# Kernel optimization log

Measured on AMD Instinct MI355X. Metric: run time of the kernel, lower is better.

## Reference

```python
import jax, jax.numpy as jnp
import numpy as np
import math

# HMS 10-20 montage probe ordering and bipolar probe groups
PROBES = ["Fp1","F3","C3","P3","F7","T3","T5","O1","Fz","Cz","Pz",
          "Fp2","F4","C4","P4","F8","T4","T6","O2","EKG"]
PROBE2IDX = {p: i for i, p in enumerate(PROBES)}
PROBE_GROUPS = {
    "LL": ["Fp1","F7","T3","T5","O1"],
    "LP": ["Fp1","F3","C3","P3","O1"],
    "RP": ["Fp2","F8","T4","T6","O2"],
    "RL": ["Fp2","F4","C4","P4","O2"],
    "Z":  ["Fz","Cz","Pz"],
}
_pairs = []
for _, probes in PROBE_GROUPS.items():
    for p1, p2 in zip(probes[:-1], probes[1:]):
        _pairs.append((PROBE2IDX[p1], PROBE2IDX[p2]))
P1_IDX = np.array([p for p, _ in _pairs])  # (18,)
P2_IDX = np.array([q for _, q in _pairs])  # (18,)

SAMPLING_RATE = 40.0
HP_CUTOFF = 0.5
LP_CUTOFF = 50.0
Q = 0.7071067811865476  # torchaudio default

def _highpass_coeffs(sr, fc, q=Q):
    w0 = 2.0 * math.pi * fc / sr
    alpha = math.sin(w0) / (2.0 * q)
    c = math.cos(w0)
    b0, b1, b2 = (1 + c) / 2, -(1 + c), (1 + c) / 2
    a0, a1, a2 = 1 + alpha, -2 * c, 1 - alpha
    return (b0 / a0, b1 / a0, b2 / a0, a1 / a0, a2 / a0)

def _lowpass_coeffs(sr, fc, q=Q):
    w0 = 2.0 * math.pi * fc / sr
    alpha = math.sin(w0) / (2.0 * q)
    c = math.cos(w0)
    b0, b1, b2 = (1 - c) / 2, 1 - c, (1 - c) / 2
    a0, a1, a2 = 1 + alpha, -2 * c, 1 - alpha
    return (b0 / a0, b1 / a0, b2 / a0, a1 / a0, a2 / a0)

def _biquad(x, coeffs):
    # x: (B, C, T); direct-form-I IIR with zero initial conditions (as torchaudio lfilter)
    b0, b1, b2, a1, a2 = coeffs
    xT = jnp.moveaxis(x, -1, 0)  # (T, B, C)
    z = jnp.zeros_like(xT[0])
    def step(carry, xn):
        x1, x2, y1, y2 = carry
        yn = b0 * xn + b1 * x1 + b2 * x2 - a1 * y1 - a2 * y2
        return (xn, x1, yn, y1), yn
    _, yT = jax.lax.scan(step, (z, z, z, z), xT)
    return jnp.moveaxis(yT, 0, -1)

def setup_inputs() -> dict:
    key = jax.random.key(0)
    k1, k2 = jax.random.split(key)
    B, T, P = 128, 16384, 20
    x = jax.random.normal(k1, (B, T, P), dtype=jnp.float32)
    mask = jax.random.uniform(k2, (B, T, P), dtype=jnp.float32)
    return {"x": x, "mask": mask}

def reference(x, mask):
    # bipolar channel differences + pair masks, then (B, C=18, T)
    x_diff = x[..., P1_IDX] - x[..., P2_IDX]          # (B, T, 18)
    pair_mask = mask[..., P1_IDX] * mask[..., P2_IDX] # (B, T, 18)
    eegs = jnp.transpose(x_diff * pair_mask, (0, 2, 1))      # apply_mask=True -> (B, 18, T)
    eeg_masks = jnp.transpose(pair_mask, (0, 2, 1))          # (B, 18, T)
    eegs = _biquad(eegs, _highpass_coeffs(SAMPLING_RATE, HP_CUTOFF))
    eegs = _biquad(eegs, _lowpass_coeffs(SAMPLING_RATE, LP_CUTOFF))
    return eegs, eeg_masks
```

## Files before the change

kernel.cpp:

```cpp
#include <hip/hip_runtime.h>
#include <math.h>

#ifndef M_PI
#define M_PI 3.14159265358979323846
#endif

#define BB     128
#define TT     16384
#define PP     20
#define NCH    18
#define EMIT   512
#define HIST   160
#define WIN    (HIST + EMIT)
#define NQ     6
#define NTAPS  (HIST + 16)
#define SFRAGS 86
#define OPITCH 516
#define NCHUNK (TT / EMIT)
#define NTILES 36

typedef float  f32x4v __attribute__((ext_vector_type(4)));
typedef short  bf16x8 __attribute__((ext_vector_type(8)));

struct HTab { float h[NTAPS]; };

__device__ __forceinline__ uint rne16(float f) {
    uint u = __float_as_uint(f);
    return (u + 0x7fffu + ((u >> 16) & 1u)) >> 16;
}

__global__ __launch_bounds__(256, 3) void collate_fir(
    const float* __restrict__ x, const float* __restrict__ msk,
    float* __restrict__ out, HTab ht)
{
    __shared__ alignas(16) ushort vhi[SFRAGS * NCH * 8];
    __shared__ alignas(16) ushort pml[NCH * OPITCH];
    __shared__ float hlds[NTAPS];

    int tid   = threadIdx.x;
    int blk   = blockIdx.x;
    int chunk = blk & (NCHUNK - 1);
    int b     = blk >> 5;
    int t0    = chunk * EMIT;

    for (int e = tid; e < 2 * NCH * 8; e += 256)
        vhi[84 * NCH * 8 + e] = 0;

    if (tid == 0) {
#pragma unroll
        for (int j = 0; j < NTAPS; ++j) hlds[j] = ht.h[j];
    }

    const float* xb   = x   + (size_t)b * TT * PP;
    const float* mb   = msk + (size_t)b * TT * PP;
    float*       oute = out;
    float*       outm = out + (size_t)BB * NCH * TT;

    constexpr int P1[NCH] = {0,4,5,6,  0,1,2,3,  11,15,16,17, 11,12,13,14, 8,9};
    constexpr int P2[NCH] = {4,5,6,7,  1,2,3,7,  15,16,17,18, 12,13,14,18, 9,10};

    for (int u = tid; u < WIN / 2; u += 256) {
        int r0   = 2 * u;
        int trow = t0 - HIST + r0;
        float xr0[PP], mr0[PP], xr1[PP], mr1[PP];
        if (trow >= 0) {
            const f32x4v* xp = reinterpret_cast<const f32x4v*>(xb + (size_t)trow * PP);
            const f32x4v* mp = reinterpret_cast<const f32x4v*>(mb + (size_t)trow * PP);
#pragma unroll
            for (int j = 0; j < 5; ++j) {
                f32x4v a0 = xp[j],     m0 = mp[j];
                f32x4v a1 = xp[5 + j], m1 = mp[5 + j];
                xr0[4*j+0]=a0.x; xr0[4*j+1]=a0.y; xr0[4*j+2]=a0.z; xr0[4*j+3]=a0.w;
                mr0[4*j+0]=m0.x; mr0[4*j+1]=m0.y; mr0[4*j+2]=m0.z; mr0[4*j+3]=m0.w;
                xr1[4*j+0]=a1.x; xr1[4*j+1]=a1.y; xr1[4*j+2]=a1.z; xr1[4*j+3]=a1.w;
                mr1[4*j+0]=m1.x; mr1[4*j+1]=m1.y; mr1[4*j+2]=m1.z; mr1[4*j+3]=m1.w;
            }
        } else {
#pragma unroll
            for (int j = 0; j < PP; ++j) { xr0[j]=0.f; mr0[j]=0.f; xr1[j]=0.f; mr1[j]=0.f; }
        }
        int  s  = r0 >> 3;
        int  e  = r0 & 7;
        bool ep = (r0 >= HIST);
#pragma unroll
        for (int c = 0; c < NCH; ++c) {
            float pm0 = mr0[P1[c]] * mr0[P2[c]];
            float pm1 = mr1[P1[c]] * mr1[P2[c]];
            float v0  = (xr0[P1[c]] - xr0[P2[c]]) * pm0;
            float v1  = (xr1[P1[c]] - xr1[P2[c]]) * pm1;
            *reinterpret_cast<uint*>(&vhi[(s * NCH + c) * 8 + e]) =
                rne16(v0) | (rne16(v1) << 16);
            if (ep)
                *reinterpret_cast<uint*>(&pml[c * OPITCH + (r0 - HIST)]) =
                    rne16(pm0) | (rne16(pm1) << 16);
        }
    }

    __syncthreads();

    int lane = tid & 63;
    int wid  = tid >> 6;
    int i16  = lane & 15;
    int g    = lane >> 4;

    bf16x8 Ah[NQ], Al[NQ];
#pragma unroll
    for (int q = 0; q < NQ; ++q) {
#pragma unroll
        for (int e = 0; e < 8; ++e) {
            int   k  = i16 + HIST - 32 * q - (g * 8 + e);
            float hv = (k >= 0 && k < NTAPS) ? hlds[k] : 0.f;
            uint  hh = rne16(hv);
            uint  hl = rne16(hv - __uint_as_float(hh << 16));
            Ah[q][e] = (short)hh;
            Al[q][e] = (short)hl;
        }
    }

    for (int e = tid; e < NCH * EMIT / 4; e += 256) {
        int c  = e >> 7;
        int tq = e & 127;
        uint2 two = *reinterpret_cast<const uint2*>(&pml[c * OPITCH + 4 * tq]);
        f32x4v o;
        o.x = __uint_as_float((two.x & 0xffffu) << 16);
        o.y = __uint_as_float(two.x & 0xffff0000u);
        o.z = __uint_as_float((two.y & 0xffffu) << 16);
        o.w = __uint_as_float(two.y & 0xffff0000u);
        *reinterpret_cast<f32x4v*>(outm + ((size_t)b * NCH + c) * TT + t0 + 4 * tq) = o;
    }

    for (int tile = wid; tile < NTILES; tile += 4) {
        int n = i16;
        int c, Tl;
        if (tile < 32) { c = n;             Tl = tile * 16; }
        else           { c = 16 + (n >> 3); Tl = (tile - 32) * 128 + (n & 7) * 16; }

        f32x4v acc = {0.f, 0.f, 0.f, 0.f};
#pragma unroll
        for (int q = 0; q < NQ; ++q) {
            int sidx = (Tl >> 3) + 4 * q + g;
            int fo   = (sidx * NCH + c) * 8;
            bf16x8 Bh = *reinterpret_cast<bf16x8*>(&vhi[fo]);
            acc = __builtin_amdgcn_mfma_f32_16x16x32_bf16(Ah[q], Bh, acc, 0, 0, 0);
            acc = __builtin_amdgcn_mfma_f32_16x16x32_bf16(Al[q], Bh, acc, 0, 0, 0);
        }
        *reinterpret_cast<f32x4v*>(oute + ((size_t)b * NCH + c) * TT + t0 + Tl + g * 4) = acc;
    }
}

extern "C" void kernel_launch(void* const* d_in, const int* in_sizes, int n_in,
                              void* d_out, int out_size, void* d_ws, size_t ws_size,
                              hipStream_t stream)
{
    const float* x = (const float*)d_in[0];
    const float* m = (const float*)d_in[1];
    float* out = (float*)d_out;

    const double sr = 40.0, q = 0.7071067811865476;
    double w0h = 2.0 * M_PI * 0.5 / sr;
    double alh = sin(w0h) / (2.0 * q), cwh = cos(w0h), a0h = 1.0 + alh;
    double b0h = ((1.0 + cwh) * 0.5) / a0h, b1h = (-(1.0 + cwh)) / a0h, b2h = b0h;
    double a1h = (-2.0 * cwh) / a0h,        a2h = (1.0 - alh) / a0h;
    double w0l = 2.0 * M_PI * 50.0 / sr;
    double all = sin(w0l) / (2.0 * q), cwl = cos(w0l), a0l = 1.0 + all;
    double b0l = ((1.0 - cwl) * 0.5) / a0l, b1l = (1.0 - cwl) / a0l, b2l = b0l;
    double a1l = (-2.0 * cwl) / a0l,        a2l = (1.0 - all) / a0l;

    HTab ht;
    {
        double hx1=0, hx2=0, hy1=0, hy2=0, lx1=0, lx2=0, ly1=0, ly2=0;
        for (int t = 0; t < NTAPS; ++t) {
            double u  = (t == 0) ? 1.0 : 0.0;
            double hy = b0h*u + b1h*hx1 + b2h*hx2 - a1h*hy1 - a2h*hy2;
            hx2 = hx1; hx1 = u;  hy2 = hy1; hy1 = hy;
            double ly = b0l*hy + b1l*lx1 + b2l*lx2 - a1l*ly1 - a2l*ly2;
            lx2 = lx1; lx1 = hy; ly2 = ly1; ly1 = ly;
            ht.h[t] = (float)ly;
        }
    }

    int grid = BB * NCHUNK;
    collate_fir<<<grid, 256, 0, stream>>>(x, m, out, ht);
}
```

Measured before the change: 149.8 us.

## Split window staging into two phases to overlap global loads with MFMA compute

The input window is staged in two parts. The first 416 rows are converted into LDS before the first barrier, and the last 256 rows are loaded into registers early. They are then written to LDS only after the first 15 MFMA tiles and half the mask output, which overlaps the tail loads with compute and stores. A second barrier gates the remaining tiles and mask output. Occupancy in launch bounds drops from 3 to 2 blocks per SM to make room for the extra live registers, which may reduce latency hiding elsewhere.

```diff
diff --git a/kernel.cpp b/kernel.cpp
--- a/kernel.cpp
+++ b/kernel.cpp
@@ -12,12 +12,14 @@
 #define EMIT   512
 #define HIST   160
 #define WIN    (HIST + EMIT)
+#define H1     416
 #define NQ     6
 #define NTAPS  (HIST + 16)
 #define SFRAGS 86
 #define OPITCH 516
 #define NCHUNK (TT / EMIT)
 #define NTILES 36
+#define TSPLIT 15
 
 typedef float  f32x4v __attribute__((ext_vector_type(4)));
 typedef short  bf16x8 __attribute__((ext_vector_type(8)));
@@ -29,7 +31,7 @@
     return (u + 0x7fffu + ((u >> 16) & 1u)) >> 16;
 }
 
-__global__ __launch_bounds__(256, 3) void collate_fir(
+__global__ __launch_bounds__(256, 2) void collate_fir(
     const float* __restrict__ x, const float* __restrict__ msk,
     float* __restrict__ out, HTab ht)
 {
@@ -45,7 +47,6 @@
 
     for (int e = tid; e < 2 * NCH * 8; e += 256)
         vhi[84 * NCH * 8 + e] = 0;
-
     if (tid == 0) {
 #pragma unroll
         for (int j = 0; j < NTAPS; ++j) hlds[j] = ht.h[j];
@@ -59,7 +60,7 @@
     constexpr int P1[NCH] = {0,4,5,6,  0,1,2,3,  11,15,16,17, 11,12,13,14, 8,9};
     constexpr int P2[NCH] = {4,5,6,7,  1,2,3,7,  15,16,17,18, 12,13,14,18, 9,10};
 
-    for (int u = tid; u < WIN / 2; u += 256) {
+    for (int u = tid; u < H1 / 2; u += 256) {
         int r0   = 2 * u;
         int trow = t0 - HIST + r0;
         float xr0[PP], mr0[PP], xr1[PP], mr1[PP];
@@ -98,6 +99,16 @@
 
     __syncthreads();
 
+    int row2  = H1 + tid;
+    int trow2 = t0 - HIST + row2;
+    f32x4v xl[5], ml[5];
+    {
+        const f32x4v* xp = reinterpret_cast<const f32x4v*>(xb + (size_t)trow2 * PP);
+        const f32x4v* mp = reinterpret_cast<const f32x4v*>(mb + (size_t)trow2 * PP);
+#pragma unroll
+        for (int j = 0; j < 5; ++j) { xl[j] = xp[j]; ml[j] = mp[j]; }
+    }
+
     int lane = tid & 63;
     int wid  = tid >> 6;
     int i16  = lane & 15;
@@ -117,9 +128,24 @@
         }
     }
 
-    for (int e = tid; e < NCH * EMIT / 4; e += 256) {
-        int c  = e >> 7;
-        int tq = e & 127;
+    for (int tile = wid; tile < TSPLIT; tile += 4) {
+        int n = i16;
+        int c = n, Tl = tile * 16;
+        f32x4v acc = {0.f, 0.f, 0.f, 0.f};
+#pragma unroll
+        for (int q = 0; q < NQ; ++q) {
+            int sidx = (Tl >> 3) + 4 * q + g;
+            int fo   = (sidx * NCH + c) * 8;
+            bf16x8 Bh = *reinterpret_cast<bf16x8*>(&vhi[fo]);
+            acc = __builtin_amdgcn_mfma_f32_16x16x32_bf16(Ah[q], Bh, acc, 0, 0, 0);
+            acc = __builtin_amdgcn_mfma_f32_16x16x32_bf16(Al[q], Bh, acc, 0, 0, 0);
+        }
+        *reinterpret_cast<f32x4v*>(oute + ((size_t)b * NCH + c) * TT + t0 + Tl + g * 4) = acc;
+    }
+
+    for (int e = tid; e < NCH * 64; e += 256) {
+        int c  = e >> 6;
+        int tq = e & 63;
         uint2 two = *reinterpret_cast<const uint2*>(&pml[c * OPITCH + 4 * tq]);
         f32x4v o;
         o.x = __uint_as_float((two.x & 0xffffu) << 16);
@@ -129,12 +155,42 @@
         *reinterpret_cast<f32x4v*>(outm + ((size_t)b * NCH + c) * TT + t0 + 4 * tq) = o;
     }
 
-    for (int tile = wid; tile < NTILES; tile += 4) {
+    {
+        float xr[PP], mr[PP];
+#pragma unroll
+        for (int j = 0; j < 5; ++j) {
+            xr[4*j+0]=xl[j].x; xr[4*j+1]=xl[j].y; xr[4*j+2]=xl[j].z; xr[4*j+3]=xl[j].w;
+            mr[4*j+0]=ml[j].x; mr[4*j+1]=ml[j].y; mr[4*j+2]=ml[j].z; mr[4*j+3]=ml[j].w;
+        }
+        int fb = ((row2 >> 3) * NCH) * 8 + (row2 & 7);
+#pragma unroll
+        for (int c = 0; c < NCH; ++c) {
+            float pm = mr[P1[c]] * mr[P2[c]];
+            float v  = (xr[P1[c]] - xr[P2[c]]) * pm;
+            vhi[fb + c * 8] = (ushort)rne16(v);
+            pml[c * OPITCH + (row2 - HIST)] = (ushort)rne16(pm);
+        }
+    }
+
+    __syncthreads();
+
+    for (int e = tid; e < NCH * 64; e += 256) {
+        int c  = e >> 6;
+        int tq = e & 63;
+        uint2 two = *reinterpret_cast<const uint2*>(&pml[c * OPITCH + 256 + 4 * tq]);
+        f32x4v o;
+        o.x = __uint_as_float((two.x & 0xffffu) << 16);
+        o.y = __uint_as_float(two.x & 0xffff0000u);
+        o.z = __uint_as_float((two.y & 0xffffu) << 16);
+        o.w = __uint_as_float(two.y & 0xffff0000u);
+        *reinterpret_cast<f32x4v*>(outm + ((size_t)b * NCH + c) * TT + t0 + 256 + 4 * tq) = o;
+    }
+
+    for (int tile = TSPLIT + wid; tile < NTILES; tile += 4) {
         int n = i16;
         int c, Tl;
         if (tile < 32) { c = n;             Tl = tile * 16; }
         else           { c = 16 + (n >> 3); Tl = (tile - 32) * 128 + (n & 7) * 16; }
-
         f32x4v acc = {0.f, 0.f, 0.f, 0.f};
 #pragma unroll
         for (int q = 0; q < NQ; ++q) {
```

After: 146.4 us. 1.02x faster.

## Stage input rows through LDS with coalesced loads and 512-thread blocks

Applied to the files above, without the earlier changes.

Replaces the per-thread strided row loads of x and mask with a cooperative coalesced vector load into a shared-memory staging buffer (stored as bf16), then computes bipolar differences per row from shared memory. Block size doubles to 512 threads with 8 waves sharing the MFMA tiles. This targets poor global-load coalescing, but adds a large LDS buffer that may reduce blocks per CU, and rounds raw inputs to bf16 before differencing, adding numerical error.

```diff
diff --git a/kernel.cpp b/kernel.cpp
--- a/kernel.cpp
+++ b/kernel.cpp
@@ -18,9 +18,11 @@
 #define OPITCH 516
 #define NCHUNK (TT / EMIT)
 #define NTILES 36
+#define RPITCH 44
 
 typedef float  f32x4v __attribute__((ext_vector_type(4)));
 typedef short  bf16x8 __attribute__((ext_vector_type(8)));
+typedef ushort u16x4  __attribute__((ext_vector_type(4)));
 
 struct HTab { float h[NTAPS]; };
 
@@ -28,11 +30,15 @@
     uint u = __float_as_uint(f);
     return (u + 0x7fffu + ((u >> 16) & 1u)) >> 16;
 }
+__device__ __forceinline__ float bf2f(uint h) {
+    return __uint_as_float(h << 16);
+}
 
-__global__ __launch_bounds__(256, 3) void collate_fir(
+__global__ __launch_bounds__(512, 2) void collate_fir(
     const float* __restrict__ x, const float* __restrict__ msk,
     float* __restrict__ out, HTab ht)
 {
+    __shared__ alignas(16) ushort raw[WIN * RPITCH];
     __shared__ alignas(16) ushort vhi[SFRAGS * NCH * 8];
     __shared__ alignas(16) ushort pml[NCH * OPITCH];
     __shared__ float hlds[NTAPS];
@@ -43,60 +49,59 @@
     int b     = blk >> 5;
     int t0    = chunk * EMIT;
 
-    for (int e = tid; e < 2 * NCH * 8; e += 256)
-        vhi[84 * NCH * 8 + e] = 0;
-
+    if (tid < 2 * NCH * 8) vhi[84 * NCH * 8 + tid] = 0;
     if (tid == 0) {
 #pragma unroll
         for (int j = 0; j < NTAPS; ++j) hlds[j] = ht.h[j];
     }
 
-    const float* xb   = x   + (size_t)b * TT * PP;
-    const float* mb   = msk + (size_t)b * TT * PP;
-    float*       oute = out;
-    float*       outm = out + (size_t)BB * NCH * TT;
+    const f32x4v* gx4 = reinterpret_cast<const f32x4v*>(x   + (size_t)b * TT * PP);
+    const f32x4v* gm4 = reinterpret_cast<const f32x4v*>(msk + (size_t)b * TT * PP);
+    float*        oute = out;
+    float*        outm = out + (size_t)BB * NCH * TT;
+
+    int gbase4 = (t0 - HIST) * (PP / 4);
+    for (int i = tid; i < WIN * (PP / 4); i += 512) {
+        int row = i / 5;
+        int c4  = (i - row * 5) * 4;
+        int g4  = gbase4 + i;
+        f32x4v a = {0.f, 0.f, 0.f, 0.f}, m = {0.f, 0.f, 0.f, 0.f};
+        if (g4 >= 0) { a = gx4[g4]; m = gm4[g4]; }
+        u16x4 pa = { (ushort)rne16(a.x), (ushort)rne16(a.y),
+                     (ushort)rne16(a.z), (ushort)rne16(a.w) };
+        u16x4 pm = { (ushort)rne16(m.x), (ushort)rne16(m.y),
+                     (ushort)rne16(m.z), (ushort)rne16(m.w) };
+        *reinterpret_cast<u16x4*>(&raw[row * RPITCH + c4])      = pa;
+        *reinterpret_cast<u16x4*>(&raw[row * RPITCH + PP + c4]) = pm;
+    }
+
+    __syncthreads();
 
     constexpr int P1[NCH] = {0,4,5,6,  0,1,2,3,  11,15,16,17, 11,12,13,14, 8,9};
     constexpr int P2[NCH] = {4,5,6,7,  1,2,3,7,  15,16,17,18, 12,13,14,18, 9,10};
 
-    for (int u = tid; u < WIN / 2; u += 256) {
-        int r0   = 2 * u;
-        int trow = t0 - HIST + r0;
-        float xr0[PP], mr0[PP], xr1[PP], mr1[PP];
-        if (trow >= 0) {
-            const f32x4v* xp = reinterpret_cast<const f32x4v*>(xb + (size_t)trow * PP);
-            const f32x4v* mp = reinterpret_cast<const f32x4v*>(mb + (size_t)trow * PP);
+    for (int r = tid; r < WIN; r += 512) {
+        float xr[PP], mr[PP];
 #pragma unroll
-            for (int j = 0; j < 5; ++j) {
-                f32x4v a0 = xp[j],     m0 = mp[j];
-                f32x4v a1 = xp[5 + j], m1 = mp[5 + j];
-                xr0[4*j+0]=a0.x; xr0[4*j+1]=a0.y; xr0[4*j+2]=a0.z; xr0[4*j+3]=a0.w;
-                mr0[4*j+0]=m0.x; mr0[4*j+1]=m0.y; mr0[4*j+2]=m0.z; mr0[4*j+3]=m0.w;
-                xr1[4*j+0]=a1.x; xr1[4*j+1]=a1.y; xr1[4*j+2]=a1.z; xr1[4*j+3]=a1.w;
-                mr1[4*j+0]=m1.x; mr1[4*j+1]=m1.y; mr1[4*j+2]=m1.z; mr1[4*j+3]=m1.w;
+        for (int j = 0; j < 5; ++j) {
+            u16x4 ux = *reinterpret_cast<const u16x4*>(&raw[r * RPITCH + 4 * j]);
+            u16x4 um = *reinterpret_cast<const u16x4*>(&raw[r * RPITCH + PP + 4 * j]);
+#pragma unroll
+            for (int k = 0; k < 4; ++k) {
+                xr[4*j+k] = bf2f(ux[k]);
+                mr[4*j+k] = bf2f(um[k]);
             }
-        } else {
-#pragma unroll
-            for (int j = 0; j < PP; ++j) { xr0[j]=0.f; mr0[j]=0.f; xr1[j]=0.f; mr1[j]=0.f; }
         }
-        int  s  = r0 >> 3;
-        int  e  = r0 & 7;
-        bool ep = (r0 >= HIST);
+        int  fb = ((r >> 3) * NCH) * 8 + (r & 7);
+        bool ep = (r >= HIST);
 #pragma unroll
         for (int c = 0; c < NCH; ++c) {
-            float pm0 = mr0[P1[c]] * mr0[P2[c]];
-            float pm1 = mr1[P1[c]] * mr1[P2[c]];
-            float v0  = (xr0[P1[c]] - xr0[P2[c]]) * pm0;
-            float v1  = (xr1[P1[c]] - xr1[P2[c]]) * pm1;
-            *reinterpret_cast<uint*>(&vhi[(s * NCH + c) * 8 + e]) =
-                rne16(v0) | (rne16(v1) << 16);
-            if (ep)
-                *reinterpret_cast<uint*>(&pml[c * OPITCH + (r0 - HIST)]) =
-                    rne16(pm0) | (rne16(pm1) << 16);
+            float pm = mr[P1[c]] * mr[P2[c]];
+            float v  = (xr[P1[c]] - xr[P2[c]]) * pm;
+            vhi[fb + c * 8] = (ushort)rne16(v);
+            if (ep) pml[c * OPITCH + (r - HIST)] = (ushort)rne16(pm);
         }
     }
-
-    __syncthreads();
 
     int lane = tid & 63;
     int wid  = tid >> 6;
@@ -111,13 +116,15 @@
             int   k  = i16 + HIST - 32 * q - (g * 8 + e);
             float hv = (k >= 0 && k < NTAPS) ? hlds[k] : 0.f;
             uint  hh = rne16(hv);
-            uint  hl = rne16(hv - __uint_as_float(hh << 16));
+            uint  hl = rne16(hv - bf2f(hh));
             Ah[q][e] = (short)hh;
             Al[q][e] = (short)hl;
         }
     }
 
-    for (int e = tid; e < NCH * EMIT / 4; e += 256) {
+    __syncthreads();
+
+    for (int e = tid; e < NCH * EMIT / 4; e += 512) {
         int c  = e >> 7;
         int tq = e & 127;
         uint2 two = *reinterpret_cast<const uint2*>(&pml[c * OPITCH + 4 * tq]);
@@ -129,7 +136,7 @@
         *reinterpret_cast<f32x4v*>(outm + ((size_t)b * NCH + c) * TT + t0 + 4 * tq) = o;
     }
 
-    for (int tile = wid; tile < NTILES; tile += 4) {
+    for (int tile = wid; tile < NTILES; tile += 8) {
         int n = i16;
         int c, Tl;
         if (tile < 32) { c = n;             Tl = tile * 16; }
@@ -180,5 +187,5 @@
     }
 
     int grid = BB * NCHUNK;
-    collate_fir<<<grid, 256, 0, stream>>>(x, m, out, ht);
+    collate_fir<<<grid, 512, 0, stream>>>(x, m, out, ht);
 }
```

Result: slower. 213.0 us (+42.1%).
